# Optimization experiments

Measured on AMD Instinct MI355X. Metric: run time of the kernel, lower is better.

Reference implementation:

```python
import jax, jax.numpy as jnp
import numpy as np

N_WORDS, N_BOOKS, L_WORD = 256, 8, 64
TAU_SQ = 5.0
B = 32768


def setup_inputs() -> dict:
    key = jax.random.key(0)
    ks = jax.random.split(key, 4)
    f = jax.random.normal(ks[0], (B, N_BOOKS * L_WORD), jnp.float32)
    # codebooks: xavier_uniform over (N_words, N_books*L_word)
    lim_c = float(np.sqrt(6.0 / (N_WORDS + N_BOOKS * L_WORD)))
    codebooks = jax.random.uniform(ks[1], (N_WORDS, N_BOOKS * L_WORD), jnp.float32, -lim_c, lim_c)
    # mlp[0]: Linear(L_word, 4*L_word), weights ~ N(0, 0.01)
    W1 = jax.random.normal(ks[2], (L_WORD, 4 * L_WORD), jnp.float32) * 0.01
    b1 = jnp.zeros((4 * L_WORD,), jnp.float32)
    # mlp[2]: Linear(4*L_word, N_books), xavier_uniform
    lim2 = float(np.sqrt(6.0 / (4 * L_WORD + N_BOOKS)))
    W2 = jax.random.uniform(ks[3], (4 * L_WORD, N_BOOKS), jnp.float32, -lim2, lim2)
    b2 = jnp.zeros((N_BOOKS,), jnp.float32)
    return dict(f=f, codebooks=codebooks, W1=W1, b1=b1, W2=W2, b2=b2)


def reference(f, codebooks, W1, b1, W2, b2):
    Bsz = f.shape[0]
    # --- soft_quantization: per-book squared distances -> softmax -> weighted codewords ---
    x = f.reshape(Bsz, N_BOOKS, L_WORD)               # (B, K, L)
    c = codebooks.reshape(N_WORDS, N_BOOKS, L_WORD)   # (W, K, L)
    # squared euclidean distance per book: (B, K, W)
    d = (jnp.sum(x * x, axis=-1)[:, :, None]
         - 2.0 * jnp.einsum('bkl,wkl->bkw', x, c)
         + jnp.sum(c * c, axis=-1).T[None, :, :])
    p = jax.nn.softmax(-TAU_SQ * d, axis=-1)          # (B, K, W) soft assignments
    z = jnp.einsum('bkw,wkl->bkl', p, c).reshape(Bsz, N_BOOKS * L_WORD)
    p_flat = p.reshape(Bsz, N_BOOKS * N_WORDS)        # concat over books along dim 1
    # --- codebook-index classifier MLP on per-book splits ---
    f_split = f.reshape(-1, L_WORD)                   # (B*K, L)
    h = jax.nn.relu(f_split @ W1 + b1)                # (B*K, 4L)
    logits_codebook = jax.nn.log_softmax(h @ W2 + b2, axis=1)  # (B*K, N_books)
    return f, z, p_flat, logits_codebook
```

## Files before the change

### kernel.cpp

```cpp
#include <hip/hip_runtime.h>

typedef __fp16   pk16x2 __attribute__((ext_vector_type(2)));
typedef _Float16 f16x8 __attribute__((ext_vector_type(8)));
typedef float    f32x4  __attribute__((ext_vector_type(4)));
typedef float    f32x16 __attribute__((ext_vector_type(16)));

static constexpr int BSZ = 32768;
static constexpr int NB  = 8;
static constexpr int NW  = 256;
static constexpr int LW  = 64;
static constexpr int DF  = 512;
#define TAU   5.0f
#define LOG2E 1.44269504088896f
#define LN2   0.69314718055994f

union U2 { pk16x2 h; unsigned u; };
union U8 { f16x8 v; unsigned u[4]; };
union F4 { f32x4 v; float a[4]; };

__device__ inline unsigned pku(float a, float b) {
    U2 c; c.h = __builtin_amdgcn_cvt_pkrtz(a, b); return c.u;
}

static constexpr size_t WS_CBH = 0;
static constexpr size_t WS_CBT = 262144;
static constexpr size_t WS_CC  = 524288;
static constexpr size_t WS_W1H = 532480;
static constexpr size_t WS_W2H = 565248;

__global__ __launch_bounds__(256) void prep_kernel(
    const float* __restrict__ cb, const float* __restrict__ W1,
    const float* __restrict__ W2, char* __restrict__ ws)
{
    _Float16* cbh = (_Float16*)(ws + WS_CBH);
    _Float16* cbt = (_Float16*)(ws + WS_CBT);
    float*    cc  = (float*)   (ws + WS_CC);
    _Float16* w1h = (_Float16*)(ws + WS_W1H);
    _Float16* w2h = (_Float16*)(ws + WS_W2H);
    const int b = blockIdx.x, t = threadIdx.x;

    if (b < 8) {
        const float* src = cb + (size_t)t * DF + b * LW;
        float c_[64];
        #pragma unroll
        for (int i = 0; i < 16; ++i)
            *(f32x4*)&c_[i * 4] = *(const f32x4*)(src + i * 4);
        float s = 0.f;
        #pragma unroll
        for (int l = 0; l < 64; ++l) s += c_[l] * c_[l];
        cc[b * 256 + t] = s;
        #pragma unroll
        for (int c8 = 0; c8 < 8; ++c8) {
            U8 u;
            #pragma unroll
            for (int m = 0; m < 4; ++m)
                u.u[m] = pku(c_[c8 * 8 + 2 * m], c_[c8 * 8 + 2 * m + 1]);
            *(f16x8*)&cbh[((size_t)(b * 256 + t)) * 64 + c8 * 8] = u.v;
        }
        #pragma unroll
        for (int l = 0; l < 64; ++l)
            cbt[((size_t)(b * 64 + l)) * 256 + t] = (_Float16)c_[l];
    } else {
        float wv[64];
        #pragma unroll
        for (int l = 0; l < 64; ++l) wv[l] = W1[l * 256 + t];
        #pragma unroll
        for (int c8 = 0; c8 < 8; ++c8) {
            U8 u;
            #pragma unroll
            for (int m = 0; m < 4; ++m)
                u.u[m] = pku(wv[c8 * 8 + 2 * m], wv[c8 * 8 + 2 * m + 1]);
            *(f16x8*)&w1h[(size_t)t * 64 + c8 * 8] = u.v;
        }
        const int c = t >> 5, h0 = (t & 31) * 8;
        #pragma unroll
        for (int j = 0; j < 8; ++j)
            w2h[c * 256 + h0 + j] = (_Float16)W2[(h0 + j) * 8 + c];
    }
}

__global__ __launch_bounds__(256, 2) void quant_kernel(
    const float* __restrict__ f, const char* __restrict__ ws,
    float* __restrict__ out_f, float* __restrict__ out_z,
    float* __restrict__ out_p)
{
    __shared__ _Float16 ct [NW * LW];
    __shared__ _Float16 ctt[LW * NW];
    __shared__ float    ccs[NW];

    const _Float16* cbh = (const _Float16*)(ws + WS_CBH);
    const _Float16* cbt = (const _Float16*)(ws + WS_CBT);
    const float*    ccw = (const float*)   (ws + WS_CC);

    const int k    = blockIdx.y;
    const int tid  = threadIdx.x;
    const int wid  = tid >> 6;
    const int lane = tid & 63;
    const int lr   = lane & 31;
    const int hi   = lane >> 5;
    const int r0   = blockIdx.x * 128;
    const int row  = r0 + wid * 32 + lr;

    #pragma unroll
    for (int it = 0; it < 8; ++it) {
        int i = it * 256 + tid;
        int w = i >> 3, s = i & 7;
        f16x8 v = *(const f16x8*)(cbh + (size_t)k * 16384 + w * 64 + s * 8);
        *(f16x8*)&ct[w * 64 + (s ^ (w & 7)) * 8] = v;
    }
    #pragma unroll
    for (int it = 0; it < 8; ++it) {
        int i = it * 256 + tid;
        int l = i >> 5, cw = i & 31;
        f16x8 v = *(const f16x8*)(cbt + (size_t)k * 16384 + l * 256 + cw * 8);
        *(f16x8*)&ctt[l * 256 + (cw ^ (l & 7)) * 8] = v;
    }
    ccs[tid] = ccw[k * 256 + tid];
    __syncthreads();

    float x_[32];
    {
        const float* fr = f     + (size_t)row * DF + k * LW + hi * 8;
        float*       fo = out_f + (size_t)row * DF + k * LW + hi * 8;
        #pragma unroll
        for (int i = 0; i < 8; ++i) {
            f32x4 v = *(const f32x4*)(fr + (i >> 1) * 16 + (i & 1) * 4);
            *(f32x4*)&x_[i * 4] = v;
            *(f32x4*)(fo + (i >> 1) * 16 + (i & 1) * 4) = v;
        }
    }
    f16x8 bxh[4];
    #pragma unroll
    for (int ks = 0; ks < 4; ++ks) {
        U8 uh;
        #pragma unroll
        for (int m = 0; m < 4; ++m)
            uh.u[m] = pku(x_[ks * 8 + 2 * m], x_[ks * 8 + 2 * m + 1]);
        bxh[ks] = uh.v;
    }

    f32x16 acc[8];
    #pragma unroll
    for (int wt = 0; wt < 8; ++wt) acc[wt] = {};
    #pragma unroll
    for (int wt = 0; wt < 8; ++wt) {
        const int w = wt * 32 + lr;
        #pragma unroll
        for (int ks = 0; ks < 4; ++ks) {
            f16x8 a = *(const f16x8*)&ct[w * 64 + (((ks * 2 + hi) ^ (lr & 7))) * 8];
            acc[wt] = __builtin_amdgcn_mfma_f32_32x32x16_f16(a, bxh[ks], acc[wt], 0, 0, 0);
        }
    }

    const float KK = TAU * LOG2E;
    float mx = -1e30f;
    #pragma unroll
    for (int wt = 0; wt < 8; ++wt) {
        #pragma unroll
        for (int g = 0; g < 4; ++g) {
            F4 cc4; cc4.v = *(const f32x4*)&ccs[wt * 32 + g * 8 + hi * 4];
            #pragma unroll
            for (int j = 0; j < 4; ++j) {
                int q = g * 4 + j;
                float li = (2.f * acc[wt][q] - cc4.a[j]) * KK;
                acc[wt][q] = li;
                mx = fmaxf(mx, li);
            }
        }
    }
    mx = fmaxf(mx, __shfl_xor(mx, 32));
    float s = 0.f;
    #pragma unroll
    for (int wt = 0; wt < 8; ++wt) {
        #pragma unroll
        for (int q = 0; q < 16; ++q) {
            float e = __builtin_amdgcn_exp2f(acc[wt][q] - mx);
            acc[wt][q] = e; s += e;
        }
    }
    s += __shfl_xor(s, 32);
    const float inv = 1.f / s;
    #pragma unroll
    for (int wt = 0; wt < 8; ++wt) {
        #pragma unroll
        for (int q = 0; q < 16; ++q) acc[wt][q] *= inv;
    }

    float* prow = out_p + (size_t)row * (NB * NW) + (size_t)k * NW + hi * 8;
    f32x16 zacc[2];
    zacc[0] = {}; zacc[1] = {};
    #pragma unroll
    for (int ks = 0; ks < 16; ++ks) {
        const int wt = ks >> 1;
        const int q0 = (ks & 1) * 8;
        float v[8];
        #pragma unroll
        for (int i = 0; i < 4; ++i) {
            float a0 = acc[wt][q0 + i];
            float a1 = acc[wt][q0 + 4 + i];
            float snd = hi ? a0 : a1;
            float rcv = __shfl_xor(snd, 32);
            v[i]     = hi ? rcv : a0;
            v[4 + i] = hi ? a1 : rcv;
        }
        *(f32x4*)(prow + ks * 16)     = f32x4{v[0], v[1], v[2], v[3]};
        *(f32x4*)(prow + ks * 16 + 4) = f32x4{v[4], v[5], v[6], v[7]};
        U8 pa;
        pa.u[0] = pku(v[0], v[1]); pa.u[1] = pku(v[2], v[3]);
        pa.u[2] = pku(v[4], v[5]); pa.u[3] = pku(v[6], v[7]);
        #pragma unroll
        for (int nt = 0; nt < 2; ++nt) {
            f16x8 bz = *(const f16x8*)&ctt[(nt * 32 + lr) * 256 + (((ks * 2 + hi) ^ (lr & 7))) * 8];
            zacc[nt] = __builtin_amdgcn_mfma_f32_32x32x16_f16(pa.v, bz, zacc[nt], 0, 0, 0);
        }
    }
    const int rbase = r0 + wid * 32;
    #pragma unroll
    for (int nt = 0; nt < 2; ++nt) {
        #pragma unroll
        for (int q = 0; q < 16; ++q) {
            int rr = (q & 3) + 8 * (q >> 2) + 4 * hi;
            out_z[(size_t)(rbase + rr) * DF + k * LW + nt * 32 + lr] = zacc[nt][q];
        }
    }
}

__global__ __launch_bounds__(256, 3) void mlp_kernel(
    const float* __restrict__ f, const char* __restrict__ ws,
    const float* __restrict__ b1, const float* __restrict__ b2,
    float* __restrict__ out_lg)
{
    __shared__ _Float16 w1t[NW * LW];
    __shared__ _Float16 w2t[8 * NW];
    __shared__ float    b1s[NW];

    const _Float16* w1h = (const _Float16*)(ws + WS_W1H);
    const _Float16* w2h = (const _Float16*)(ws + WS_W2H);

    const int tid  = threadIdx.x;
    const int wid  = tid >> 6;
    const int lane = tid & 63;
    const int lr   = lane & 31;
    const int hi   = lane >> 5;
    const int m0   = blockIdx.x * 128;
    const int m    = m0 + wid * 32 + lr;

    #pragma unroll
    for (int it = 0; it < 8; ++it) {
        int i = it * 256 + tid;
        int h = i >> 3, s = i & 7;
        f16x8 v = *(const f16x8*)(w1h + h * 64 + s * 8);
        *(f16x8*)&w1t[h * 64 + (s ^ (h & 7)) * 8] = v;
    }
    {
        int mm = tid >> 5, c = tid & 31;
        f16x8 v = *(const f16x8*)(w2h + mm * 256 + c * 8);
        *(f16x8*)&w2t[mm * 256 + (c ^ mm) * 8] = v;
    }
    b1s[tid] = b1[tid];
    __syncthreads();

    float x_[32];
    {
        const float* fr = f + (size_t)m * LW + hi * 8;
        #pragma unroll
        for (int i = 0; i < 8; ++i)
            *(f32x4*)&x_[i * 4] = *(const f32x4*)(fr + (i >> 1) * 16 + (i & 1) * 4);
    }
    f16x8 bxh[4];
    #pragma unroll
    for (int ks = 0; ks < 4; ++ks) {
        U8 uh;
        #pragma unroll
        for (int mm = 0; mm < 4; ++mm)
            uh.u[mm] = pku(x_[ks * 8 + 2 * mm], x_[ks * 8 + 2 * mm + 1]);
        bxh[ks] = uh.v;
    }

    f32x16 acc2 = {};
    #pragma unroll
    for (int ht = 0; ht < 8; ++ht) {
        f32x16 a1 = {};
        #pragma unroll
        for (int ks = 0; ks < 4; ++ks) {
            f16x8 a = *(const f16x8*)&w1t[(ht * 32 + lr) * 64 + (((ks * 2 + hi) ^ (lr & 7))) * 8];
            a1 = __builtin_amdgcn_mfma_f32_32x32x16_f16(a, bxh[ks], a1, 0, 0, 0);
        }
        float hv[16];
        #pragma unroll
        for (int g = 0; g < 4; ++g) {
            F4 b4; b4.v = *(const f32x4*)&b1s[ht * 32 + g * 8 + hi * 4];
            #pragma unroll
            for (int j = 0; j < 4; ++j) {
                int q = g * 4 + j;
                hv[q] = fmaxf(a1[q] + b4.a[j], 0.f);
            }
        }
        #pragma unroll
        for (int half = 0; half < 2; ++half) {
            const int ks = 2 * ht + half;
            const int q0 = half * 8;
            float v[8];
            #pragma unroll
            for (int i = 0; i < 4; ++i) {
                float a0 = hv[q0 + i];
                float a1v = hv[q0 + 4 + i];
                float snd = hi ? a0 : a1v;
                float rcv = __shfl_xor(snd, 32);
                v[i]     = hi ? rcv : a0;
                v[4 + i] = hi ? a1v : rcv;
            }
            U8 hb;
            hb.u[0] = pku(v[0], v[1]); hb.u[1] = pku(v[2], v[3]);
            hb.u[2] = pku(v[4], v[5]); hb.u[3] = pku(v[6], v[7]);
            f16x8 aw2 = *(const f16x8*)&w2t[(lr & 7) * 256 + (((ks * 2 + hi) ^ (lr & 7))) * 8];
            acc2 = __builtin_amdgcn_mfma_f32_32x32x16_f16(aw2, hb.v, acc2, 0, 0, 0);
        }
    }

    F4 b2v; b2v.v = *(const f32x4*)(b2 + hi * 4);
    float lg[4];
    #pragma unroll
    for (int q = 0; q < 4; ++q) lg[q] = acc2[q] + b2v.a[q];
    float mm = fmaxf(fmaxf(lg[0], lg[1]), fmaxf(lg[2], lg[3]));
    mm = fmaxf(mm, __shfl_xor(mm, 32));
    float se = 0.f;
    #pragma unroll
    for (int q = 0; q < 4; ++q) se += __builtin_amdgcn_exp2f((lg[q] - mm) * LOG2E);
    se += __shfl_xor(se, 32);
    float lse = mm + __builtin_amdgcn_logf(se) * LN2;
    *(f32x4*)(out_lg + (size_t)m * 8 + hi * 4) =
        f32x4{lg[0] - lse, lg[1] - lse, lg[2] - lse, lg[3] - lse};
}

extern "C" void kernel_launch(void* const* d_in, const int* in_sizes, int n_in,
                              void* d_out, int out_size, void* d_ws, size_t ws_size,
                              hipStream_t stream) {
    const float* f  = (const float*)d_in[0];
    const float* cb = (const float*)d_in[1];
    const float* W1 = (const float*)d_in[2];
    const float* b1 = (const float*)d_in[3];
    const float* W2 = (const float*)d_in[4];
    const float* b2 = (const float*)d_in[5];

    float* out    = (float*)d_out;
    float* out_f  = out;
    float* out_z  = out_f + (size_t)BSZ * DF;
    float* out_p  = out_z + (size_t)BSZ * DF;
    float* out_lg = out_p + (size_t)BSZ * NB * NW;

    hipLaunchKernelGGL(prep_kernel, dim3(9), dim3(256), 0, stream,
                       cb, W1, W2, (char*)d_ws);
    hipLaunchKernelGGL(quant_kernel, dim3(BSZ / 128, NB), dim3(256), 0, stream,
                       f, (const char*)d_ws, out_f, out_z, out_p);
    hipLaunchKernelGGL(mlp_kernel, dim3(BSZ * NB / 128), dim3(256), 0, stream,
                       f, (const char*)d_ws, b1, b2, out_lg);
}
```

Before: 163.0 us.

## Merge quant and MLP kernels into one launch with interleaved block roles

Merges the soft-quantization kernel and the MLP classifier kernel into a single kernel. Even x-blocks run the quantization path and odd x-blocks run the MLP path, sharing one raw LDS buffer. The aim is to remove a launch and the tail/serialization gap between the two kernels by letting both workloads run on the GPU at the same time. In exchange, the MLP blocks now take on the larger LDS allocation and the 2-blocks-per-SM launch bound of the quant path, which may lower their occupancy.

```diff
diff --git a/kernel.cpp b/kernel.cpp
--- a/kernel.cpp
+++ b/kernel.cpp
@@ -79,258 +79,254 @@
     }
 }
 
-__global__ __launch_bounds__(256, 2) void quant_kernel(
+__global__ __launch_bounds__(256, 2) void mega_kernel(
     const float* __restrict__ f, const char* __restrict__ ws,
+    const float* __restrict__ b1, const float* __restrict__ b2,
     float* __restrict__ out_f, float* __restrict__ out_z,
-    float* __restrict__ out_p)
+    float* __restrict__ out_p, float* __restrict__ out_lg)
 {
-    __shared__ _Float16 ct [NW * LW];
-    __shared__ _Float16 ctt[LW * NW];
-    __shared__ float    ccs[NW];
-
-    const _Float16* cbh = (const _Float16*)(ws + WS_CBH);
-    const _Float16* cbt = (const _Float16*)(ws + WS_CBT);
-    const float*    ccw = (const float*)   (ws + WS_CC);
-
-    const int k    = blockIdx.y;
+    __shared__ __align__(16) char lds[66560];
+
     const int tid  = threadIdx.x;
     const int wid  = tid >> 6;
     const int lane = tid & 63;
     const int lr   = lane & 31;
     const int hi   = lane >> 5;
-    const int r0   = blockIdx.x * 128;
-    const int row  = r0 + wid * 32 + lr;
-
-    #pragma unroll
-    for (int it = 0; it < 8; ++it) {
-        int i = it * 256 + tid;
-        int w = i >> 3, s = i & 7;
-        f16x8 v = *(const f16x8*)(cbh + (size_t)k * 16384 + w * 64 + s * 8);
-        *(f16x8*)&ct[w * 64 + (s ^ (w & 7)) * 8] = v;
-    }
-    #pragma unroll
-    for (int it = 0; it < 8; ++it) {
-        int i = it * 256 + tid;
-        int l = i >> 5, cw = i & 31;
-        f16x8 v = *(const f16x8*)(cbt + (size_t)k * 16384 + l * 256 + cw * 8);
-        *(f16x8*)&ctt[l * 256 + (cw ^ (l & 7)) * 8] = v;
-    }
-    ccs[tid] = ccw[k * 256 + tid];
-    __syncthreads();
-
-    float x_[32];
-    {
-        const float* fr = f     + (size_t)row * DF + k * LW + hi * 8;
-        float*       fo = out_f + (size_t)row * DF + k * LW + hi * 8;
-        #pragma unroll
-        for (int i = 0; i < 8; ++i) {
-            f32x4 v = *(const f32x4*)(fr + (i >> 1) * 16 + (i & 1) * 4);
-            *(f32x4*)&x_[i * 4] = v;
-            *(f32x4*)(fo + (i >> 1) * 16 + (i & 1) * 4) = v;
-        }
-    }
-    f16x8 bxh[4];
-    #pragma unroll
-    for (int ks = 0; ks < 4; ++ks) {
-        U8 uh;
-        #pragma unroll
-        for (int m = 0; m < 4; ++m)
-            uh.u[m] = pku(x_[ks * 8 + 2 * m], x_[ks * 8 + 2 * m + 1]);
-        bxh[ks] = uh.v;
-    }
-
-    f32x16 acc[8];
-    #pragma unroll
-    for (int wt = 0; wt < 8; ++wt) acc[wt] = {};
-    #pragma unroll
-    for (int wt = 0; wt < 8; ++wt) {
-        const int w = wt * 32 + lr;
+
+    if ((blockIdx.x & 1) == 0) {
+        _Float16* ct  = (_Float16*)lds;
+        _Float16* ctt = (_Float16*)(lds + 32768);
+        float*    ccs = (float*)   (lds + 65536);
+
+        const _Float16* cbh = (const _Float16*)(ws + WS_CBH);
+        const _Float16* cbt = (const _Float16*)(ws + WS_CBT);
+        const float*    ccw = (const float*)   (ws + WS_CC);
+
+        const int k   = blockIdx.y;
+        const int r0  = (blockIdx.x >> 1) * 128;
+        const int row = r0 + wid * 32 + lr;
+
+        #pragma unroll
+        for (int it = 0; it < 8; ++it) {
+            int i = it * 256 + tid;
+            int w = i >> 3, s = i & 7;
+            f16x8 v = *(const f16x8*)(cbh + (size_t)k * 16384 + w * 64 + s * 8);
+            *(f16x8*)&ct[w * 64 + (s ^ (w & 7)) * 8] = v;
+        }
+        #pragma unroll
+        for (int it = 0; it < 8; ++it) {
+            int i = it * 256 + tid;
+            int l = i >> 5, cw = i & 31;
+            f16x8 v = *(const f16x8*)(cbt + (size_t)k * 16384 + l * 256 + cw * 8);
+            *(f16x8*)&ctt[l * 256 + (cw ^ (l & 7)) * 8] = v;
+        }
+        ccs[tid] = ccw[k * 256 + tid];
+        __syncthreads();
+
+        float x_[32];
+        {
+            const float* fr = f     + (size_t)row * DF + k * LW + hi * 8;
+            float*       fo = out_f + (size_t)row * DF + k * LW + hi * 8;
+            #pragma unroll
+            for (int i = 0; i < 8; ++i) {
+                f32x4 v = *(const f32x4*)(fr + (i >> 1) * 16 + (i & 1) * 4);
+                *(f32x4*)&x_[i * 4] = v;
+                *(f32x4*)(fo + (i >> 1) * 16 + (i & 1) * 4) = v;
+            }
+        }
+        f16x8 bxh[4];
         #pragma unroll
         for (int ks = 0; ks < 4; ++ks) {
-            f16x8 a = *(const f16x8*)&ct[w * 64 + (((ks * 2 + hi) ^ (lr & 7))) * 8];
-            acc[wt] = __builtin_amdgcn_mfma_f32_32x32x16_f16(a, bxh[ks], acc[wt], 0, 0, 0);
-        }
-    }
-
-    const float KK = TAU * LOG2E;
-    float mx = -1e30f;
-    #pragma unroll
-    for (int wt = 0; wt < 8; ++wt) {
-        #pragma unroll
-        for (int g = 0; g < 4; ++g) {
-            F4 cc4; cc4.v = *(const f32x4*)&ccs[wt * 32 + g * 8 + hi * 4];
-            #pragma unroll
-            for (int j = 0; j < 4; ++j) {
-                int q = g * 4 + j;
-                float li = (2.f * acc[wt][q] - cc4.a[j]) * KK;
-                acc[wt][q] = li;
-                mx = fmaxf(mx, li);
-            }
-        }
-    }
-    mx = fmaxf(mx, __shfl_xor(mx, 32));
-    float s = 0.f;
-    #pragma unroll
-    for (int wt = 0; wt < 8; ++wt) {
-        #pragma unroll
-        for (int q = 0; q < 16; ++q) {
-            float e = __builtin_amdgcn_exp2f(acc[wt][q] - mx);
-            acc[wt][q] = e; s += e;
-        }
-    }
-    s += __shfl_xor(s, 32);
-    const float inv = 1.f / s;
-    #pragma unroll
-    for (int wt = 0; wt < 8; ++wt) {
-        #pragma unroll
-        for (int q = 0; q < 16; ++q) acc[wt][q] *= inv;
-    }
-
-    float* prow = out_p + (size_t)row * (NB * NW) + (size_t)k * NW + hi * 8;
-    f32x16 zacc[2];
-    zacc[0] = {}; zacc[1] = {};
-    #pragma unroll
-    for (int ks = 0; ks < 16; ++ks) {
-        const int wt = ks >> 1;
-        const int q0 = (ks & 1) * 8;
-        float v[8];
-        #pragma unroll
-        for (int i = 0; i < 4; ++i) {
-            float a0 = acc[wt][q0 + i];
-            float a1 = acc[wt][q0 + 4 + i];
-            float snd = hi ? a0 : a1;
-            float rcv = __shfl_xor(snd, 32);
-            v[i]     = hi ? rcv : a0;
-            v[4 + i] = hi ? a1 : rcv;
-        }
-        *(f32x4*)(prow + ks * 16)     = f32x4{v[0], v[1], v[2], v[3]};
-        *(f32x4*)(prow + ks * 16 + 4) = f32x4{v[4], v[5], v[6], v[7]};
-        U8 pa;
-        pa.u[0] = pku(v[0], v[1]); pa.u[1] = pku(v[2], v[3]);
-        pa.u[2] = pku(v[4], v[5]); pa.u[3] = pku(v[6], v[7]);
-        #pragma unroll
-        for (int nt = 0; nt < 2; ++nt) {
-            f16x8 bz = *(const f16x8*)&ctt[(nt * 32 + lr) * 256 + (((ks * 2 + hi) ^ (lr & 7))) * 8];
-            zacc[nt] = __builtin_amdgcn_mfma_f32_32x32x16_f16(pa.v, bz, zacc[nt], 0, 0, 0);
-        }
-    }
-    const int rbase = r0 + wid * 32;
-    #pragma unroll
-    for (int nt = 0; nt < 2; ++nt) {
-        #pragma unroll
-        for (int q = 0; q < 16; ++q) {
-            int rr = (q & 3) + 8 * (q >> 2) + 4 * hi;
-            out_z[(size_t)(rbase + rr) * DF + k * LW + nt * 32 + lr] = zacc[nt][q];
-        }
-    }
-}
-
-__global__ __launch_bounds__(256, 3) void mlp_kernel(
-    const float* __restrict__ f, const char* __restrict__ ws,
-    const float* __restrict__ b1, const float* __restrict__ b2,
-    float* __restrict__ out_lg)
-{
-    __shared__ _Float16 w1t[NW * LW];
-    __shared__ _Float16 w2t[8 * NW];
-    __shared__ float    b1s[NW];
-
-    const _Float16* w1h = (const _Float16*)(ws + WS_W1H);
-    const _Float16* w2h = (const _Float16*)(ws + WS_W2H);
-
-    const int tid  = threadIdx.x;
-    const int wid  = tid >> 6;
-    const int lane = tid & 63;
-    const int lr   = lane & 31;
-    const int hi   = lane >> 5;
-    const int m0   = blockIdx.x * 128;
-    const int m    = m0 + wid * 32 + lr;
-
-    #pragma unroll
-    for (int it = 0; it < 8; ++it) {
-        int i = it * 256 + tid;
-        int h = i >> 3, s = i & 7;
-        f16x8 v = *(const f16x8*)(w1h + h * 64 + s * 8);
-        *(f16x8*)&w1t[h * 64 + (s ^ (h & 7)) * 8] = v;
-    }
-    {
-        int mm = tid >> 5, c = tid & 31;
-        f16x8 v = *(const f16x8*)(w2h + mm * 256 + c * 8);
-        *(f16x8*)&w2t[mm * 256 + (c ^ mm) * 8] = v;
-    }
-    b1s[tid] = b1[tid];
-    __syncthreads();
-
-    float x_[32];
-    {
-        const float* fr = f + (size_t)m * LW + hi * 8;
-        #pragma unroll
-        for (int i = 0; i < 8; ++i)
-            *(f32x4*)&x_[i * 4] = *(const f32x4*)(fr + (i >> 1) * 16 + (i & 1) * 4);
-    }
-    f16x8 bxh[4];
-    #pragma unroll
-    for (int ks = 0; ks < 4; ++ks) {
-        U8 uh;
-        #pragma unroll
-        for (int mm = 0; mm < 4; ++mm)
-            uh.u[mm] = pku(x_[ks * 8 + 2 * mm], x_[ks * 8 + 2 * mm + 1]);
-        bxh[ks] = uh.v;
-    }
-
-    f32x16 acc2 = {};
-    #pragma unroll
-    for (int ht = 0; ht < 8; ++ht) {
-        f32x16 a1 = {};
-        #pragma unroll
-        for (int ks = 0; ks < 4; ++ks) {
-            f16x8 a = *(const f16x8*)&w1t[(ht * 32 + lr) * 64 + (((ks * 2 + hi) ^ (lr & 7))) * 8];
-            a1 = __builtin_amdgcn_mfma_f32_32x32x16_f16(a, bxh[ks], a1, 0, 0, 0);
-        }
-        float hv[16];
-        #pragma unroll
-        for (int g = 0; g < 4; ++g) {
-            F4 b4; b4.v = *(const f32x4*)&b1s[ht * 32 + g * 8 + hi * 4];
-            #pragma unroll
-            for (int j = 0; j < 4; ++j) {
-                int q = g * 4 + j;
-                hv[q] = fmaxf(a1[q] + b4.a[j], 0.f);
-            }
-        }
-        #pragma unroll
-        for (int half = 0; half < 2; ++half) {
-            const int ks = 2 * ht + half;
-            const int q0 = half * 8;
+            U8 uh;
+            #pragma unroll
+            for (int m = 0; m < 4; ++m)
+                uh.u[m] = pku(x_[ks * 8 + 2 * m], x_[ks * 8 + 2 * m + 1]);
+            bxh[ks] = uh.v;
+        }
+
+        f32x16 acc[8];
+        #pragma unroll
+        for (int wt = 0; wt < 8; ++wt) acc[wt] = {};
+        #pragma unroll
+        for (int wt = 0; wt < 8; ++wt) {
+            const int w = wt * 32 + lr;
+            #pragma unroll
+            for (int ks = 0; ks < 4; ++ks) {
+                f16x8 a = *(const f16x8*)&ct[w * 64 + (((ks * 2 + hi) ^ (lr & 7))) * 8];
+                acc[wt] = __builtin_amdgcn_mfma_f32_32x32x16_f16(a, bxh[ks], acc[wt], 0, 0, 0);
+            }
+        }
+
+        const float KK = TAU * LOG2E;
+        float mx = -1e30f;
+        #pragma unroll
+        for (int wt = 0; wt < 8; ++wt) {
+            #pragma unroll
+            for (int g = 0; g < 4; ++g) {
+                F4 cc4; cc4.v = *(const f32x4*)&ccs[wt * 32 + g * 8 + hi * 4];
+                #pragma unroll
+                for (int j = 0; j < 4; ++j) {
+                    int q = g * 4 + j;
+                    float li = (2.f * acc[wt][q] - cc4.a[j]) * KK;
+                    acc[wt][q] = li;
+                    mx = fmaxf(mx, li);
+                }
+            }
+        }
+        mx = fmaxf(mx, __shfl_xor(mx, 32));
+        float s = 0.f;
+        #pragma unroll
+        for (int wt = 0; wt < 8; ++wt) {
+            #pragma unroll
+            for (int q = 0; q < 16; ++q) {
+                float e = __builtin_amdgcn_exp2f(acc[wt][q] - mx);
+                acc[wt][q] = e; s += e;
+            }
+        }
+        s += __shfl_xor(s, 32);
+        const float inv = 1.f / s;
+        #pragma unroll
+        for (int wt = 0; wt < 8; ++wt) {
+            #pragma unroll
+            for (int q = 0; q < 16; ++q) acc[wt][q] *= inv;
+        }
+
+        float* prow = out_p + (size_t)row * (NB * NW) + (size_t)k * NW + hi * 8;
+        f32x16 zacc[2];
+        zacc[0] = {}; zacc[1] = {};
+        #pragma unroll
+        for (int ks = 0; ks < 16; ++ks) {
+            const int wt = ks >> 1;
+            const int q0 = (ks & 1) * 8;
             float v[8];
             #pragma unroll
             for (int i = 0; i < 4; ++i) {
-                float a0 = hv[q0 + i];
-                float a1v = hv[q0 + 4 + i];
-                float snd = hi ? a0 : a1v;
+                float a0 = acc[wt][q0 + i];
+                float a1 = acc[wt][q0 + 4 + i];
+                float snd = hi ? a0 : a1;
                 float rcv = __shfl_xor(snd, 32);
                 v[i]     = hi ? rcv : a0;
-                v[4 + i] = hi ? a1v : rcv;
-            }
-            U8 hb;
-            hb.u[0] = pku(v[0], v[1]); hb.u[1] = pku(v[2], v[3]);
-            hb.u[2] = pku(v[4], v[5]); hb.u[3] = pku(v[6], v[7]);
-            f16x8 aw2 = *(const f16x8*)&w2t[(lr & 7) * 256 + (((ks * 2 + hi) ^ (lr & 7))) * 8];
-            acc2 = __builtin_amdgcn_mfma_f32_32x32x16_f16(aw2, hb.v, acc2, 0, 0, 0);
-        }
+                v[4 + i] = hi ? a1 : rcv;
+            }
+            *(f32x4*)(prow + ks * 16)     = f32x4{v[0], v[1], v[2], v[3]};
+            *(f32x4*)(prow + ks * 16 + 4) = f32x4{v[4], v[5], v[6], v[7]};
+            U8 pa;
+            pa.u[0] = pku(v[0], v[1]); pa.u[1] = pku(v[2], v[3]);
+            pa.u[2] = pku(v[4], v[5]); pa.u[3] = pku(v[6], v[7]);
+            #pragma unroll
+            for (int nt = 0; nt < 2; ++nt) {
+                f16x8 bz = *(const f16x8*)&ctt[(nt * 32 + lr) * 256 + (((ks * 2 + hi) ^ (lr & 7))) * 8];
+                zacc[nt] = __builtin_amdgcn_mfma_f32_32x32x16_f16(pa.v, bz, zacc[nt], 0, 0, 0);
+            }
+        }
+        const int rbase = r0 + wid * 32;
+        #pragma unroll
+        for (int nt = 0; nt < 2; ++nt) {
+            #pragma unroll
+            for (int q = 0; q < 16; ++q) {
+                int rr = (q & 3) + 8 * (q >> 2) + 4 * hi;
+                out_z[(size_t)(rbase + rr) * DF + k * LW + nt * 32 + lr] = zacc[nt][q];
+            }
+        }
+    } else {
+        _Float16* w1t = (_Float16*)lds;
+        _Float16* w2t = (_Float16*)(lds + 32768);
+        float*    b1s = (float*)   (lds + 36864);
+
+        const _Float16* w1h = (const _Float16*)(ws + WS_W1H);
+        const _Float16* w2h = (const _Float16*)(ws + WS_W2H);
+
+        const int bid = (blockIdx.x >> 1) * 8 + blockIdx.y;
+        const int m0  = bid * 128;
+        const int m   = m0 + wid * 32 + lr;
+
+        #pragma unroll
+        for (int it = 0; it < 8; ++it) {
+            int i = it * 256 + tid;
+            int h = i >> 3, s = i & 7;
+            f16x8 v = *(const f16x8*)(w1h + h * 64 + s * 8);
+            *(f16x8*)&w1t[h * 64 + (s ^ (h & 7)) * 8] = v;
+        }
+        {
+            int mm = tid >> 5, c = tid & 31;
+            f16x8 v = *(const f16x8*)(w2h + mm * 256 + c * 8);
+            *(f16x8*)&w2t[mm * 256 + (c ^ mm) * 8] = v;
+        }
+        b1s[tid] = b1[tid];
+        __syncthreads();
+
+        float x_[32];
+        {
+            const float* fr = f + (size_t)m * LW + hi * 8;
+            #pragma unroll
+            for (int i = 0; i < 8; ++i)
+                *(f32x4*)&x_[i * 4] = *(const f32x4*)(fr + (i >> 1) * 16 + (i & 1) * 4);
+        }
+        f16x8 bxh[4];
+        #pragma unroll
+        for (int ks = 0; ks < 4; ++ks) {
+            U8 uh;
+            #pragma unroll
+            for (int mm = 0; mm < 4; ++mm)
+                uh.u[mm] = pku(x_[ks * 8 + 2 * mm], x_[ks * 8 + 2 * mm + 1]);
+            bxh[ks] = uh.v;
+        }
+
+        f32x16 acc2 = {};
+        #pragma unroll
+        for (int ht = 0; ht < 8; ++ht) {
+            f32x16 a1 = {};
+            #pragma unroll
+            for (int ks = 0; ks < 4; ++ks) {
+                f16x8 a = *(const f16x8*)&w1t[(ht * 32 + lr) * 64 + (((ks * 2 + hi) ^ (lr & 7))) * 8];
+                a1 = __builtin_amdgcn_mfma_f32_32x32x16_f16(a, bxh[ks], a1, 0, 0, 0);
+            }
+            float hv[16];
+            #pragma unroll
+            for (int g = 0; g < 4; ++g) {
+                F4 b4; b4.v = *(const f32x4*)&b1s[ht * 32 + g * 8 + hi * 4];
+                #pragma unroll
+                for (int j = 0; j < 4; ++j) {
+                    int q = g * 4 + j;
+                    hv[q] = fmaxf(a1[q] + b4.a[j], 0.f);
+                }
+            }
+            #pragma unroll
+            for (int half = 0; half < 2; ++half) {
+                const int ks = 2 * ht + half;
+                const int q0 = half * 8;
+                float v[8];
+                #pragma unroll
+                for (int i = 0; i < 4; ++i) {
+                    float a0 = hv[q0 + i];
+                    float a1v = hv[q0 + 4 + i];
+                    float snd = hi ? a0 : a1v;
+                    float rcv = __shfl_xor(snd, 32);
+                    v[i]     = hi ? rcv : a0;
+                    v[4 + i] = hi ? a1v : rcv;
+                }
+                U8 hb;
+                hb.u[0] = pku(v[0], v[1]); hb.u[1] = pku(v[2], v[3]);
+                hb.u[2] = pku(v[4], v[5]); hb.u[3] = pku(v[6], v[7]);
+                f16x8 aw2 = *(const f16x8*)&w2t[(lr & 7) * 256 + (((ks * 2 + hi) ^ (lr & 7))) * 8];
+                acc2 = __builtin_amdgcn_mfma_f32_32x32x16_f16(aw2, hb.v, acc2, 0, 0, 0);
+            }
+        }
+
+        F4 b2v; b2v.v = *(const f32x4*)(b2 + hi * 4);
+        float lg[4];
+        #pragma unroll
+        for (int q = 0; q < 4; ++q) lg[q] = acc2[q] + b2v.a[q];
+        float mm2 = fmaxf(fmaxf(lg[0], lg[1]), fmaxf(lg[2], lg[3]));
+        mm2 = fmaxf(mm2, __shfl_xor(mm2, 32));
+        float se = 0.f;
+        #pragma unroll
+        for (int q = 0; q < 4; ++q) se += __builtin_amdgcn_exp2f((lg[q] - mm2) * LOG2E);
+        se += __shfl_xor(se, 32);
+        float lse = mm2 + __builtin_amdgcn_logf(se) * LN2;
+        *(f32x4*)(out_lg + (size_t)m * 8 + hi * 4) =
+            f32x4{lg[0] - lse, lg[1] - lse, lg[2] - lse, lg[3] - lse};
     }
-
-    F4 b2v; b2v.v = *(const f32x4*)(b2 + hi * 4);
-    float lg[4];
-    #pragma unroll
-    for (int q = 0; q < 4; ++q) lg[q] = acc2[q] + b2v.a[q];
-    float mm = fmaxf(fmaxf(lg[0], lg[1]), fmaxf(lg[2], lg[3]));
-    mm = fmaxf(mm, __shfl_xor(mm, 32));
-    float se = 0.f;
-    #pragma unroll
-    for (int q = 0; q < 4; ++q) se += __builtin_amdgcn_exp2f((lg[q] - mm) * LOG2E);
-    se += __shfl_xor(se, 32);
-    float lse = mm + __builtin_amdgcn_logf(se) * LN2;
-    *(f32x4*)(out_lg + (size_t)m * 8 + hi * 4) =
-        f32x4{lg[0] - lse, lg[1] - lse, lg[2] - lse, lg[3] - lse};
 }
 
 extern "C" void kernel_launch(void* const* d_in, const int* in_sizes, int n_in,
@@ -351,8 +347,6 @@
 
     hipLaunchKernelGGL(prep_kernel, dim3(9), dim3(256), 0, stream,
                        cb, W1, W2, (char*)d_ws);
-    hipLaunchKernelGGL(quant_kernel, dim3(BSZ / 128, NB), dim3(256), 0, stream,
-                       f, (const char*)d_ws, out_f, out_z, out_p);
-    hipLaunchKernelGGL(mlp_kernel, dim3(BSZ * NB / 128), dim3(256), 0, stream,
-                       f, (const char*)d_ws, b1, b2, out_lg);
+    hipLaunchKernelGGL(mega_kernel, dim3(512, 8), dim3(256), 0, stream,
+                       f, (const char*)d_ws, b1, b2, out_f, out_z, out_p, out_lg);
 }
```

Result: slower. 178.3 us (+9.4%).

## Use online softmax with packed fp16 probabilities and larger quant blocks

Applied to the files above, without the earlier changes.

Rewrites the quant kernel's softmax as an online (running-max) softmax that packs each probability tile into fp16 right after the exponent, so the 128 fp32 accumulators no longer stay live. This lowers register pressure so the kernel can run 512-thread blocks over 256 rows at higher occupancy, sharing each codebook load in LDS across twice as many rows. The MLP kernel's occupancy hint is also raised. In exchange, the written probabilities now pass through fp16 rescaling and normalization, which reduces their precision, and there is extra rescale work on each tile.

```diff
diff --git a/kernel.cpp b/kernel.cpp
--- a/kernel.cpp
+++ b/kernel.cpp
@@ -79,7 +79,7 @@
     }
 }
 
-__global__ __launch_bounds__(256, 2) void quant_kernel(
+__global__ __launch_bounds__(512, 4) void quant_kernel(
     const float* __restrict__ f, const char* __restrict__ ws,
     float* __restrict__ out_f, float* __restrict__ out_z,
     float* __restrict__ out_p)
@@ -98,24 +98,24 @@
     const int lane = tid & 63;
     const int lr   = lane & 31;
     const int hi   = lane >> 5;
-    const int r0   = blockIdx.x * 128;
+    const int r0   = blockIdx.x * 256;
     const int row  = r0 + wid * 32 + lr;
 
     #pragma unroll
-    for (int it = 0; it < 8; ++it) {
-        int i = it * 256 + tid;
+    for (int it = 0; it < 4; ++it) {
+        int i = it * 512 + tid;
         int w = i >> 3, s = i & 7;
         f16x8 v = *(const f16x8*)(cbh + (size_t)k * 16384 + w * 64 + s * 8);
         *(f16x8*)&ct[w * 64 + (s ^ (w & 7)) * 8] = v;
     }
     #pragma unroll
-    for (int it = 0; it < 8; ++it) {
-        int i = it * 256 + tid;
+    for (int it = 0; it < 4; ++it) {
+        int i = it * 512 + tid;
         int l = i >> 5, cw = i & 31;
         f16x8 v = *(const f16x8*)(cbt + (size_t)k * 16384 + l * 256 + cw * 8);
         *(f16x8*)&ctt[l * 256 + (cw ^ (l & 7)) * 8] = v;
     }
-    ccs[tid] = ccw[k * 256 + tid];
+    if (tid < 256) ccs[tid] = ccw[k * 256 + tid];
     __syncthreads();
 
     float x_[32];
@@ -139,51 +139,68 @@
         bxh[ks] = uh.v;
     }
 
-    f32x16 acc[8];
-    #pragma unroll
-    for (int wt = 0; wt < 8; ++wt) acc[wt] = {};
+    const float KK = TAU * LOG2E;
+    f16x8 pf[16];
+    float m = -1e30f, s = 0.f;
     #pragma unroll
     for (int wt = 0; wt < 8; ++wt) {
+        f32x16 acc = {};
         const int w = wt * 32 + lr;
         #pragma unroll
         for (int ks = 0; ks < 4; ++ks) {
             f16x8 a = *(const f16x8*)&ct[w * 64 + (((ks * 2 + hi) ^ (lr & 7))) * 8];
-            acc[wt] = __builtin_amdgcn_mfma_f32_32x32x16_f16(a, bxh[ks], acc[wt], 0, 0, 0);
-        }
-    }
-
-    const float KK = TAU * LOG2E;
-    float mx = -1e30f;
-    #pragma unroll
-    for (int wt = 0; wt < 8; ++wt) {
+            acc = __builtin_amdgcn_mfma_f32_32x32x16_f16(a, bxh[ks], acc, 0, 0, 0);
+        }
+        float li[16];
+        float tm = -1e30f;
         #pragma unroll
         for (int g = 0; g < 4; ++g) {
             F4 cc4; cc4.v = *(const f32x4*)&ccs[wt * 32 + g * 8 + hi * 4];
             #pragma unroll
             for (int j = 0; j < 4; ++j) {
                 int q = g * 4 + j;
-                float li = (2.f * acc[wt][q] - cc4.a[j]) * KK;
-                acc[wt][q] = li;
-                mx = fmaxf(mx, li);
+                li[q] = (2.f * acc[q] - cc4.a[j]) * KK;
+                tm = fmaxf(tm, li[q]);
             }
         }
-    }
-    mx = fmaxf(mx, __shfl_xor(mx, 32));
-    float s = 0.f;
-    #pragma unroll
-    for (int wt = 0; wt < 8; ++wt) {
+        tm = fmaxf(tm, __shfl_xor(tm, 32));
+        float mnew = fmaxf(m, tm);
+        float r = __builtin_amdgcn_exp2f(m - mnew);
+        s *= r;
+        _Float16 r16 = (_Float16)r;
+        #pragma unroll
+        for (int t = 0; t < 2 * wt; ++t) pf[t] *= r16;
+        float e[16];
         #pragma unroll
         for (int q = 0; q < 16; ++q) {
-            float e = __builtin_amdgcn_exp2f(acc[wt][q] - mx);
-            acc[wt][q] = e; s += e;
+            e[q] = __builtin_amdgcn_exp2f(li[q] - mnew);
+            s += e[q];
+        }
+        m = mnew;
+        #pragma unroll
+        for (int half = 0; half < 2; ++half) {
+            const int q0 = half * 8;
+            float v[8];
+            #pragma unroll
+            for (int i = 0; i < 4; ++i) {
+                float a0 = e[q0 + i];
+                float a1 = e[q0 + 4 + i];
+                float snd = hi ? a0 : a1;
+                float rcv = __shfl_xor(snd, 32);
+                v[i]     = hi ? rcv : a0;
+                v[4 + i] = hi ? a1 : rcv;
+            }
+            U8 pa;
+            pa.u[0] = pku(v[0], v[1]); pa.u[1] = pku(v[2], v[3]);
+            pa.u[2] = pku(v[4], v[5]); pa.u[3] = pku(v[6], v[7]);
+            pf[2 * wt + half] = pa.v;
         }
     }
     s += __shfl_xor(s, 32);
-    const float inv = 1.f / s;
-    #pragma unroll
-    for (int wt = 0; wt < 8; ++wt) {
-        #pragma unroll
-        for (int q = 0; q < 16; ++q) acc[wt][q] *= inv;
+    {
+        _Float16 inv16 = (_Float16)(1.f / s);
+        #pragma unroll
+        for (int t = 0; t < 16; ++t) pf[t] *= inv16;
     }
 
     float* prow = out_p + (size_t)row * (NB * NW) + (size_t)k * NW + hi * 8;
@@ -191,27 +208,15 @@
     zacc[0] = {}; zacc[1] = {};
     #pragma unroll
     for (int ks = 0; ks < 16; ++ks) {
-        const int wt = ks >> 1;
-        const int q0 = (ks & 1) * 8;
-        float v[8];
-        #pragma unroll
-        for (int i = 0; i < 4; ++i) {
-            float a0 = acc[wt][q0 + i];
-            float a1 = acc[wt][q0 + 4 + i];
-            float snd = hi ? a0 : a1;
-            float rcv = __shfl_xor(snd, 32);
-            v[i]     = hi ? rcv : a0;
-            v[4 + i] = hi ? a1 : rcv;
-        }
-        *(f32x4*)(prow + ks * 16)     = f32x4{v[0], v[1], v[2], v[3]};
-        *(f32x4*)(prow + ks * 16 + 4) = f32x4{v[4], v[5], v[6], v[7]};
-        U8 pa;
-        pa.u[0] = pku(v[0], v[1]); pa.u[1] = pku(v[2], v[3]);
-        pa.u[2] = pku(v[4], v[5]); pa.u[3] = pku(v[6], v[7]);
+        f16x8 pv = pf[ks];
+        f32x4 p0 = {(float)pv[0], (float)pv[1], (float)pv[2], (float)pv[3]};
+        f32x4 p1 = {(float)pv[4], (float)pv[5], (float)pv[6], (float)pv[7]};
+        *(f32x4*)(prow + ks * 16)     = p0;
+        *(f32x4*)(prow + ks * 16 + 4) = p1;
         #pragma unroll
         for (int nt = 0; nt < 2; ++nt) {
             f16x8 bz = *(const f16x8*)&ctt[(nt * 32 + lr) * 256 + (((ks * 2 + hi) ^ (lr & 7))) * 8];
-            zacc[nt] = __builtin_amdgcn_mfma_f32_32x32x16_f16(pa.v, bz, zacc[nt], 0, 0, 0);
+            zacc[nt] = __builtin_amdgcn_mfma_f32_32x32x16_f16(pv, bz, zacc[nt], 0, 0, 0);
         }
     }
     const int rbase = r0 + wid * 32;
@@ -225,7 +230,7 @@
     }
 }
 
-__global__ __launch_bounds__(256, 3) void mlp_kernel(
+__global__ __launch_bounds__(256, 4) void mlp_kernel(
     const float* __restrict__ f, const char* __restrict__ ws,
     const float* __restrict__ b1, const float* __restrict__ b2,
     float* __restrict__ out_lg)
@@ -351,7 +356,7 @@
 
     hipLaunchKernelGGL(prep_kernel, dim3(9), dim3(256), 0, stream,
                        cb, W1, W2, (char*)d_ws);
-    hipLaunchKernelGGL(quant_kernel, dim3(BSZ / 128, NB), dim3(256), 0, stream,
+    hipLaunchKernelGGL(quant_kernel, dim3(BSZ / 256, NB), dim3(512), 0, stream,
                        f, (const char*)d_ws, out_f, out_z, out_p);
     hipLaunchKernelGGL(mlp_kernel, dim3(BSZ * NB / 128), dim3(256), 0, stream,
                        f, (const char*)d_ws, b1, b2, out_lg);
```

Result: slower. 325.3 us (+99.5%).
